# Kernel optimization log

Hardware: AMD Instinct MI355X
Metric: run time of the kernel (lower is better)

The kernel has to match this reference:

```python
import jax, jax.numpy as jnp
import numpy as np
from jax import lax


def setup_inputs() -> dict:
    key = jax.random.key(0)
    k1, k2, k3 = jax.random.split(key, 3)
    B, C_in, T, C_out = 8, 256, 4096, 256
    x = jax.random.normal(k1, (B, C_in, T), dtype=jnp.float32)
    # torch Conv1d weight: [4*out, in, kernel=2], bias: [4*out]
    fan_in = C_in * 2
    bound = 1.0 / np.sqrt(fan_in)
    W = jax.random.uniform(k2, (4 * C_out, C_in, 2), dtype=jnp.float32, minval=-bound, maxval=bound)
    b = jax.random.uniform(k3, (4 * C_out,), dtype=jnp.float32, minval=-bound, maxval=bound)
    return {"x": x, "W": W, "b": b}


def _qrnn_forward(x, W, b):
    # Conv1d(pad=1) then dropping last timestep == causal left-pad (1,0) conv, kernel 2.
    out = lax.conv_general_dilated(
        x, W, window_strides=(1,), padding=[(1, 0)],
        dimension_numbers=("NCH", "OIH", "NCH"),
    ) + b[None, :, None]  # [B, 4*out, T]
    Z, F, O, I = jnp.split(out, 4, axis=1)
    Z = jnp.tanh(Z)
    F = jax.nn.sigmoid(F)
    O = jax.nn.sigmoid(O)
    I = jax.nn.sigmoid(I)
    # Linear recurrence c_t = f_t * c_{t-1} + i_t * z_t via parallel associative scan.
    def combine(e1, e2):
        a1, b1 = e1
        a2, b2 = e2
        return (a2 * a1, a2 * b1 + b2)
    _, c = lax.associative_scan(combine, (F, I * Z), axis=2)
    return O * c  # H: [B, out, T]


def reference(x, W, b):
    return _qrnn_forward(x, W, b)
```

## Files before the change

kernel.cpp:

```cpp
#include <hip/hip_runtime.h>
#include <hip/hip_fp16.h>

#define B_   8
#define CIN  256
#define T_   4096
#define TP   4097
#define CO   256
#define O4   1024
#define NN   32768
#define NCH  128
#define CL   32

#define OFF_XF   0
#define OFF_WF   4195328
#define OFF_F16  4457472
#define OFF_IZ16 8651776
#define OFF_O16  12846080
#define OFF_A    17040384
#define OFF_B    17302528

typedef __attribute__((ext_vector_type(8))) _Float16 half8;
typedef __attribute__((ext_vector_type(4))) float floatx4;

__device__ __forceinline__ float fsig(float x)  { return 1.0f / (1.0f + __expf(-x)); }
__device__ __forceinline__ float ftanh(float x) { return 2.0f / (1.0f + __expf(-2.0f * x)) - 1.0f; }

__device__ __forceinline__ unsigned short f16b(float v) {
    return __half_as_ushort(__float2half(v));
}

__device__ __forceinline__ void glds16(const unsigned short* g, unsigned short* l) {
    __builtin_amdgcn_global_load_lds(
        (const __attribute__((address_space(1))) unsigned*)g,
        (__attribute__((address_space(3))) unsigned*)l, 16, 0, 0);
}

__global__ void convert_kernel(const float* __restrict__ W,
                               const float* __restrict__ x,
                               unsigned short* __restrict__ Wf,
                               unsigned short* __restrict__ Xf) {
    __shared__ float tile[64][69];
    const int bid = blockIdx.x;
    const int tid = threadIdx.x;
    if (bid < 2048) {
        int e = bid * 256 + tid;
        int r = e >> 9, k = e & 511;
        int g = r & 3, c = r >> 2;
        int j = k >> 8, i = k & 255;
        float v = W[((size_t)((g << 8) + c)) * 512 + i * 2 + j];
        Wf[e] = f16b(v);
        return;
    }
    const int b2 = bid - 2048;
    const int t0 = (b2 & 63) * 64;
    const int c0 = ((b2 >> 6) & 3) * 64;
    const int b  = b2 >> 8;

    {
        int j4 = (tid & 15) * 4, r16 = tid >> 4;
#pragma unroll
        for (int p = 0; p < 4; p++) {
            int i = p * 16 + r16;
            float4 v = *(const float4*)&x[((size_t)(b * 256 + c0 + i)) * T_ + t0 + j4];
            tile[i][j4] = v.x; tile[i][j4 + 1] = v.y;
            tile[i][j4 + 2] = v.z; tile[i][j4 + 3] = v.w;
        }
    }
    if (t0 == 0 && tid < 64) {
        Xf[(size_t)b * TP * 256 + c0 + tid] = 0;
    }
    __syncthreads();
    {
        const int cslot = tid & 15, trow = tid >> 4;
#pragma unroll
        for (int p = 0; p < 4; p++) {
            int t = p * 16 + trow;
            unsigned lo = (unsigned)f16b(tile[cslot * 4 + 0][t])
                        | ((unsigned)f16b(tile[cslot * 4 + 1][t]) << 16);
            unsigned hi = (unsigned)f16b(tile[cslot * 4 + 2][t])
                        | ((unsigned)f16b(tile[cslot * 4 + 3][t]) << 16);
            size_t idx = ((size_t)b * TP + t0 + t + 1) * 256 + c0 + cslot * 4;
            uint2 pk; pk.x = lo; pk.y = hi;
            *(uint2*)&Xf[idx] = pk;
        }
    }
}

__launch_bounds__(512, 6)
__global__ void gemm_mfma_kernel(const unsigned short* __restrict__ Xf,
                                 const unsigned short* __restrict__ Wf,
                                 const float* __restrict__ bias,
                                 __half* __restrict__ fw,
                                 __half* __restrict__ izw,
                                 __half* __restrict__ ow,
                                 float* __restrict__ Aw,
                                 float* __restrict__ Bw)
{
    __shared__ unsigned short smem_us[24576];

    const int tid  = threadIdx.x;
    const int wave = tid >> 6, lane = tid & 63;
    const int q = lane >> 4, mr = lane & 15;
    const int wm = wave >> 2, wn = wave & 3;

    const int bid   = blockIdx.x;
    const int xcd   = bid & 7;
    const int idx   = bid >> 3;
    const int n_blk = xcd * 32 + (idx >> 3);
    const int r_blk = idx & 7;
    const int r0 = r_blk * 128;
    const int n0 = n_blk * 128;
    const int bb = n0 >> 12;
    const int t0 = n0 & (T_ - 1);

    const int lrow = lane >> 2;
    const int lcol = (((lane & 3) ^ ((lrow >> 1) & 3)) * 8);
    const unsigned short* pW = Wf + (size_t)(r0 + wave * 16 + lrow) * 512 + lcol;
    const unsigned short* pX = Xf + ((size_t)bb * TP + t0 + wave * 16 + lrow) * 256 + lcol;

    const int swz = (q ^ ((mr >> 1) & 3)) * 8;
    const int aoffb = (wm * 64 + mr) * 32 + swz;
    const int boffb = (wn * 32 + mr) * 32 + swz;
    const int wst = wave * 512;

    floatx4 acc[4][2];
#pragma unroll
    for (int v = 0; v < 4; v++)
#pragma unroll
        for (int u = 0; u < 2; u++) acc[v][u] = (floatx4){0.f, 0.f, 0.f, 0.f};

    glds16(pW,      smem_us + wst);
    glds16(pX,      smem_us + 4096 + wst);
    glds16(pW + 32, smem_us + 8192 + wst);
    glds16(pX + 32, smem_us + 8192 + 4096 + wst);
    asm volatile("s_waitcnt vmcnt(2)" ::: "memory");
    __builtin_amdgcn_s_barrier();
    __builtin_amdgcn_sched_barrier(0);

#pragma unroll 16
    for (int i = 0; i < 16; ++i) {
        const unsigned short* Ac = smem_us + (i % 3) * 8192;
        const unsigned short* Bc = Ac + 4096;
        unsigned short* dA = smem_us + ((i + 2) % 3) * 8192 + wst;
        unsigned short* dB = dA + 4096;
        const unsigned kkn = (unsigned)(((i + 2) & 15) * 32);

        glds16(pW + kkn, dA);
        glds16(pX + kkn, dB);

        half8 ah[4], bh[2];
#pragma unroll
        for (int v = 0; v < 4; ++v) ah[v] = *(const half8*)(Ac + aoffb + v * 512);
#pragma unroll
        for (int u = 0; u < 2; ++u) bh[u] = *(const half8*)(Bc + boffb + u * 512);
        asm volatile("s_waitcnt lgkmcnt(0)" ::: "memory");
        __builtin_amdgcn_sched_barrier(0);
        __builtin_amdgcn_s_setprio(1);
#pragma unroll
        for (int v = 0; v < 4; ++v)
#pragma unroll
            for (int u = 0; u < 2; ++u)
                acc[v][u] = __builtin_amdgcn_mfma_f32_16x16x32_f16(ah[v], bh[u], acc[v][u], 0, 0, 0);
        __builtin_amdgcn_s_setprio(0);
        asm volatile("s_waitcnt vmcnt(2)" ::: "memory");
        __builtin_amdgcn_s_barrier();
        __builtin_amdgcn_sched_barrier(0);
    }

    asm volatile("s_waitcnt vmcnt(0)" ::: "memory");
    __syncthreads();
    __half* epf = (__half*)smem_us;
    __half* epz = epf + 128 * 36;
    __half* epo = epz + 128 * 36;
    const int ch_base = r0 >> 2;

#pragma unroll
    for (int v = 0; v < 4; ++v) {
        const int cl = wm * 16 + v * 4 + q;
        const int ch = ch_base + cl;
        const float bz  = bias[ch];
        const float bf_ = bias[256 + ch];
        const float bo  = bias[512 + ch];
        const float bi  = bias[768 + ch];
#pragma unroll
        for (int u = 0; u < 2; ++u) {
            const int t_l = wn * 32 + u * 16 + mr;
            float zv = ftanh(acc[v][u][0] + bz);
            float fv = fsig(acc[v][u][1] + bf_);
            float ov = fsig(acc[v][u][2] + bo);
            float iv = fsig(acc[v][u][3] + bi);
            const int off = t_l * 36 + cl;
            epf[off] = __float2half(fv);
            epz[off] = __float2half(iv * zv);
            epo[off] = __float2half(ov);
        }
    }
    __syncthreads();

    {
        const int t_r = tid >> 2;
        const int c8 = (tid & 3) << 3;
        const size_t gbase = ((size_t)bb * T_ + t0 + t_r) * 256 + ch_base + c8;
        const int lb = t_r * 36 + c8;
        union { uint2 u2[2]; uint4 u4; } pk;
        pk.u2[0] = *(const uint2*)&epf[lb];
        pk.u2[1] = *(const uint2*)&epf[lb + 4];
        *(uint4*)&fw[gbase] = pk.u4;
        pk.u2[0] = *(const uint2*)&epz[lb];
        pk.u2[1] = *(const uint2*)&epz[lb + 4];
        *(uint4*)&izw[gbase] = pk.u4;
        pk.u2[0] = *(const uint2*)&epo[lb];
        pk.u2[1] = *(const uint2*)&epo[lb + 4];
        *(uint4*)&ow[gbase] = pk.u4;
    }

    if (tid < 128) {
        const int chunk = tid >> 5;
        const int c = tid & 31;
        float A = 1.0f, Bv = 0.0f;
        const int base = (chunk * 32) * 36 + c;
#pragma unroll 4
        for (int j = 0; j < 32; ++j) {
            float f  = __half2float(epf[base + j * 36]);
            float iz = __half2float(epz[base + j * 36]);
            Bv = fmaf(f, Bv, iz);
            A *= f;
        }
        const int chunk_abs = (t0 >> 5) + chunk;
        const size_t aidx = ((size_t)bb * NCH + chunk_abs) * 256 + ch_base + c;
        Aw[aidx] = A;
        Bw[aidx] = Bv;
    }
}

__global__ void scan_phase3(const __half* __restrict__ fw, const __half* __restrict__ izw,
                            const __half* __restrict__ ow,
                            const float* __restrict__ Aw, const float* __restrict__ Bw,
                            float* __restrict__ out)
{
    __shared__ float hbuf[CL][257];
    __shared__ float carry_s[256];
    int b = blockIdx.y, ch = blockIdx.x;
    int tid = threadIdx.x;

    {
        const int c = tid;
        float carry = 0.0f;
        for (int g = 0; g < 8; ++g) {
            if (g * 16 >= ch) break;
            float Ar[16], Br[16];
#pragma unroll
            for (int j = 0; j < 16; ++j) {
                int jj = g * 16 + j;
                bool ok = jj < ch;
                size_t idx2 = ((size_t)(b * NCH + (ok ? jj : 0))) * CO + c;
                Ar[j] = ok ? Aw[idx2] : 1.0f;
                Br[j] = ok ? Bw[idx2] : 0.0f;
            }
#pragma unroll
            for (int j = 0; j < 16; ++j) carry = fmaf(Ar[j], carry, Br[j]);
        }
        carry_s[c] = carry;
    }
    __syncthreads();

    if (tid < 128) {
        const int c2 = tid * 2;
        float cs0 = carry_s[c2];
        float cs1 = carry_s[c2 + 1];
        size_t base = ((size_t)(b * T_ + ch * CL)) * CO + c2;
#pragma unroll 4
        for (int tt = 0; tt < CL; tt++) {
            __half2 f2  = *(const __half2*)&fw [base + (size_t)tt * CO];
            __half2 iz2 = *(const __half2*)&izw[base + (size_t)tt * CO];
            __half2 o2  = *(const __half2*)&ow [base + (size_t)tt * CO];
            float2 f  = __half22float2(f2);
            float2 iz = __half22float2(iz2);
            float2 o  = __half22float2(o2);
            cs0 = fmaf(f.x, cs0, iz.x);
            cs1 = fmaf(f.y, cs1, iz.y);
            hbuf[tt][c2]     = o.x * cs0;
            hbuf[tt][c2 + 1] = o.y * cs1;
        }
    }
    __syncthreads();

    {
        const int tt4 = (tid & 7) * 4;
        const int cc0 = tid >> 3;
#pragma unroll
        for (int w = 0; w < 8; ++w) {
            const int cc = cc0 + w * 32;
            float4 h4;
            h4.x = hbuf[tt4 + 0][cc];
            h4.y = hbuf[tt4 + 1][cc];
            h4.z = hbuf[tt4 + 2][cc];
            h4.w = hbuf[tt4 + 3][cc];
            *(float4*)&out[((size_t)(b * CO + cc)) * T_ + ch * CL + tt4] = h4;
        }
    }
}

extern "C" void kernel_launch(void* const* d_in, const int* in_sizes, int n_in,
                              void* d_out, int out_size, void* d_ws, size_t ws_size,
                              hipStream_t stream) {
    const float* x    = (const float*)d_in[0];
    const float* W    = (const float*)d_in[1];
    const float* bias = (const float*)d_in[2];
    float* out = (float*)d_out;
    float* ws  = (float*)d_ws;

    unsigned short* Xf = (unsigned short*)(ws + OFF_XF);
    unsigned short* Wf = (unsigned short*)(ws + OFF_WF);
    __half* fw  = (__half*)(ws + OFF_F16);
    __half* izw = (__half*)(ws + OFF_IZ16);
    __half* ow  = (__half*)(ws + OFF_O16);
    float* Aw  = ws + OFF_A;
    float* Bw  = ws + OFF_B;

    convert_kernel<<<4096, 256, 0, stream>>>(W, x, Wf, Xf);
    gemm_mfma_kernel<<<(NN / 128) * (O4 / 128), 512, 0, stream>>>(
        Xf, Wf, bias, fw, izw, ow, Aw, Bw);
    scan_phase3<<<dim3(NCH, B_), CO, 0, stream>>>(fw, izw, ow, Aw, Bw, out);
}
```

Before: 155.3 us.

## Enlarge GEMM block tile to 256 output rows per block

Doubles the GEMM block's output-row tile from 128 to 256, so each wave computes a 64x64 sub-tile (4x4 MFMAs) instead of 64x32. The LDS staging buffers, the epilogue layout with a stride of 72, and the chunk-summary pass are all resized to match, and the grid shrinks by half. The aim is more reuse of the X tile per block and more MFMA work per LDS read, cutting redundant global and LDS traffic. In exchange it uses more registers and LDS, lowers occupancy (launch bounds go from 6 to 4), and leaves fewer blocks to fill the GPU.

```diff
diff --git a/kernel.cpp b/kernel.cpp
--- a/kernel.cpp
+++ b/kernel.cpp
@@ -86,7 +86,7 @@
     }
 }
 
-__launch_bounds__(512, 6)
+__launch_bounds__(512, 4)
 __global__ void gemm_mfma_kernel(const unsigned short* __restrict__ Xf,
                                  const unsigned short* __restrict__ Wf,
                                  const float* __restrict__ bias,
@@ -96,73 +96,76 @@
                                  float* __restrict__ Aw,
                                  float* __restrict__ Bw)
 {
-    __shared__ unsigned short smem_us[24576];
+    __shared__ unsigned short smem_us[36864];
 
     const int tid  = threadIdx.x;
     const int wave = tid >> 6, lane = tid & 63;
     const int q = lane >> 4, mr = lane & 15;
-    const int wm = wave >> 2, wn = wave & 3;
+    const int wm = wave >> 1, wn = wave & 1;
 
     const int bid   = blockIdx.x;
     const int xcd   = bid & 7;
     const int idx   = bid >> 3;
-    const int n_blk = xcd * 32 + (idx >> 3);
-    const int r_blk = idx & 7;
-    const int r0 = r_blk * 128;
+    const int n_blk = xcd * 32 + (idx >> 2);
+    const int r_blk = idx & 3;
+    const int r0 = r_blk * 256;
     const int n0 = n_blk * 128;
     const int bb = n0 >> 12;
     const int t0 = n0 & (T_ - 1);
 
     const int lrow = lane >> 2;
     const int lcol = (((lane & 3) ^ ((lrow >> 1) & 3)) * 8);
-    const unsigned short* pW = Wf + (size_t)(r0 + wave * 16 + lrow) * 512 + lcol;
+    const unsigned short* pW0 = Wf + (size_t)(r0 + wave * 32 + lrow) * 512 + lcol;
+    const unsigned short* pW1 = pW0 + 16 * 512;
     const unsigned short* pX = Xf + ((size_t)bb * TP + t0 + wave * 16 + lrow) * 256 + lcol;
 
     const int swz = (q ^ ((mr >> 1) & 3)) * 8;
     const int aoffb = (wm * 64 + mr) * 32 + swz;
-    const int boffb = (wn * 32 + mr) * 32 + swz;
-    const int wst = wave * 512;
-
-    floatx4 acc[4][2];
+    const int boffb = 8192 + (wn * 64 + mr) * 32 + swz;
+    const int wstA = wave * 1024;
+    const int wstB = 8192 + wave * 512;
+
+    floatx4 acc[4][4];
 #pragma unroll
     for (int v = 0; v < 4; v++)
 #pragma unroll
-        for (int u = 0; u < 2; u++) acc[v][u] = (floatx4){0.f, 0.f, 0.f, 0.f};
-
-    glds16(pW,      smem_us + wst);
-    glds16(pX,      smem_us + 4096 + wst);
-    glds16(pW + 32, smem_us + 8192 + wst);
-    glds16(pX + 32, smem_us + 8192 + 4096 + wst);
-    asm volatile("s_waitcnt vmcnt(2)" ::: "memory");
+        for (int u = 0; u < 4; u++) acc[v][u] = (floatx4){0.f, 0.f, 0.f, 0.f};
+
+    glds16(pW0,      smem_us + wstA);
+    glds16(pW1,      smem_us + wstA + 512);
+    glds16(pX,       smem_us + wstB);
+    glds16(pW0 + 32, smem_us + 12288 + wstA);
+    glds16(pW1 + 32, smem_us + 12288 + wstA + 512);
+    glds16(pX + 32,  smem_us + 12288 + wstB);
+    asm volatile("s_waitcnt vmcnt(3)" ::: "memory");
     __builtin_amdgcn_s_barrier();
     __builtin_amdgcn_sched_barrier(0);
 
 #pragma unroll 16
     for (int i = 0; i < 16; ++i) {
-        const unsigned short* Ac = smem_us + (i % 3) * 8192;
-        const unsigned short* Bc = Ac + 4096;
-        unsigned short* dA = smem_us + ((i + 2) % 3) * 8192 + wst;
-        unsigned short* dB = dA + 4096;
+        const unsigned short* Bufc = smem_us + (i % 3) * 12288;
+        unsigned short* dbase = smem_us + ((i + 2) % 3) * 12288;
         const unsigned kkn = (unsigned)(((i + 2) & 15) * 32);
 
-        glds16(pW + kkn, dA);
-        glds16(pX + kkn, dB);
-
-        half8 ah[4], bh[2];
-#pragma unroll
-        for (int v = 0; v < 4; ++v) ah[v] = *(const half8*)(Ac + aoffb + v * 512);
-#pragma unroll
-        for (int u = 0; u < 2; ++u) bh[u] = *(const half8*)(Bc + boffb + u * 512);
+        glds16(pW0 + kkn, dbase + wstA);
+        glds16(pW1 + kkn, dbase + wstA + 512);
+        glds16(pX + kkn,  dbase + wstB);
+
+        half8 ah[4], bh[4];
+#pragma unroll
+        for (int v = 0; v < 4; ++v) ah[v] = *(const half8*)(Bufc + aoffb + v * 512);
+#pragma unroll
+        for (int u = 0; u < 4; ++u) bh[u] = *(const half8*)(Bufc + boffb + u * 512);
         asm volatile("s_waitcnt lgkmcnt(0)" ::: "memory");
         __builtin_amdgcn_sched_barrier(0);
         __builtin_amdgcn_s_setprio(1);
 #pragma unroll
         for (int v = 0; v < 4; ++v)
 #pragma unroll
-            for (int u = 0; u < 2; ++u)
+            for (int u = 0; u < 4; ++u)
                 acc[v][u] = __builtin_amdgcn_mfma_f32_16x16x32_f16(ah[v], bh[u], acc[v][u], 0, 0, 0);
         __builtin_amdgcn_s_setprio(0);
-        asm volatile("s_waitcnt vmcnt(2)" ::: "memory");
+        asm volatile("s_waitcnt vmcnt(3)" ::: "memory");
         __builtin_amdgcn_s_barrier();
         __builtin_amdgcn_sched_barrier(0);
     }
@@ -170,8 +173,8 @@
     asm volatile("s_waitcnt vmcnt(0)" ::: "memory");
     __syncthreads();
     __half* epf = (__half*)smem_us;
-    __half* epz = epf + 128 * 36;
-    __half* epo = epz + 128 * 36;
+    __half* epz = epf + 128 * 72;
+    __half* epo = epz + 128 * 72;
     const int ch_base = r0 >> 2;
 
 #pragma unroll
@@ -183,13 +186,13 @@
         const float bo  = bias[512 + ch];
         const float bi  = bias[768 + ch];
 #pragma unroll
-        for (int u = 0; u < 2; ++u) {
-            const int t_l = wn * 32 + u * 16 + mr;
+        for (int u = 0; u < 4; ++u) {
+            const int t_l = wn * 64 + u * 16 + mr;
             float zv = ftanh(acc[v][u][0] + bz);
             float fv = fsig(acc[v][u][1] + bf_);
             float ov = fsig(acc[v][u][2] + bo);
             float iv = fsig(acc[v][u][3] + bi);
-            const int off = t_l * 36 + cl;
+            const int off = t_l * 72 + cl;
             epf[off] = __float2half(fv);
             epz[off] = __float2half(iv * zv);
             epo[off] = __float2half(ov);
@@ -199,30 +202,35 @@
 
     {
         const int t_r = tid >> 2;
-        const int c8 = (tid & 3) << 3;
-        const size_t gbase = ((size_t)bb * T_ + t0 + t_r) * 256 + ch_base + c8;
-        const int lb = t_r * 36 + c8;
-        union { uint2 u2[2]; uint4 u4; } pk;
-        pk.u2[0] = *(const uint2*)&epf[lb];
-        pk.u2[1] = *(const uint2*)&epf[lb + 4];
-        *(uint4*)&fw[gbase] = pk.u4;
-        pk.u2[0] = *(const uint2*)&epz[lb];
-        pk.u2[1] = *(const uint2*)&epz[lb + 4];
-        *(uint4*)&izw[gbase] = pk.u4;
-        pk.u2[0] = *(const uint2*)&epo[lb];
-        pk.u2[1] = *(const uint2*)&epo[lb + 4];
-        *(uint4*)&ow[gbase] = pk.u4;
-    }
-
-    if (tid < 128) {
-        const int chunk = tid >> 5;
-        const int c = tid & 31;
+        const int c16 = (tid & 3) << 4;
+        const size_t gbase = ((size_t)bb * T_ + t0 + t_r) * 256 + ch_base + c16;
+        const int lb = t_r * 72 + c16;
+        {
+            const uint4* s = (const uint4*)&epf[lb];
+            uint4* d = (uint4*)&fw[gbase];
+            d[0] = s[0]; d[1] = s[1];
+        }
+        {
+            const uint4* s = (const uint4*)&epz[lb];
+            uint4* d = (uint4*)&izw[gbase];
+            d[0] = s[0]; d[1] = s[1];
+        }
+        {
+            const uint4* s = (const uint4*)&epo[lb];
+            uint4* d = (uint4*)&ow[gbase];
+            d[0] = s[0]; d[1] = s[1];
+        }
+    }
+
+    if (tid < 256) {
+        const int chunk = tid >> 6;
+        const int c = tid & 63;
         float A = 1.0f, Bv = 0.0f;
-        const int base = (chunk * 32) * 36 + c;
+        const int base = (chunk * 32) * 72 + c;
 #pragma unroll 4
         for (int j = 0; j < 32; ++j) {
-            float f  = __half2float(epf[base + j * 36]);
-            float iz = __half2float(epz[base + j * 36]);
+            float f  = __half2float(epf[base + j * 72]);
+            float iz = __half2float(epz[base + j * 72]);
             Bv = fmaf(f, Bv, iz);
             A *= f;
         }
@@ -319,7 +327,7 @@
     float* Bw  = ws + OFF_B;
 
     convert_kernel<<<4096, 256, 0, stream>>>(W, x, Wf, Xf);
-    gemm_mfma_kernel<<<(NN / 128) * (O4 / 128), 512, 0, stream>>>(
+    gemm_mfma_kernel<<<(NN / 128) * (O4 / 256), 512, 0, stream>>>(
         Xf, Wf, bias, fw, izw, ow, Aw, Bw);
     scan_phase3<<<dim3(NCH, B_), CO, 0, stream>>>(fw, izw, ow, Aw, Bw, out);
 }
```

Result: no change. 154.9 us (-0.2%).
